# Optimization experiments

Measured on AMD Instinct MI355X. Metric: run time of the kernel, lower is better.

## Reference

```python
import jax, jax.numpy as jnp
import numpy as np

SR = 44100
N_BINS = 84
BPO = 12
FMIN = 32.7
HOP = 1024


def _config():
    # Static CQT geometry (mirrors ICQT.__init__)
    Q = 1.0 / (2.0 ** (1.0 / BPO) - 1.0)
    freqs = FMIN * 2.0 ** (np.arange(N_BINS) / BPO)
    wlens = np.round(Q * SR / freqs).astype(np.int64)  # per-bin window lengths (ragged)
    return freqs, wlens


def setup_inputs() -> dict:
    key = jax.random.key(0)
    # complex CQT stacked as (nb_samples, nb_channels, n_bins, n_frames, 2)
    X = jax.random.normal(key, (4, 2, N_BINS, 256, 2), dtype=jnp.float32)
    return {"X": X}


def reference(X):
    freqs, wlens = _config()
    max_wl = int(wlens.max())
    nb_s, nb_c, n_bins, n_frames, _ = X.shape
    # default length in ICQT.forward when length is None
    length = (n_frames - 1) * HOP + max_wl

    Xf = X.reshape(-1, n_bins, n_frames, 2)
    c = (Xf[..., 0] + 1j * Xf[..., 1]).astype(jnp.complex64)  # view_as_complex
    B = c.shape[0]

    starts = np.arange(n_frames) * HOP  # static frame start times
    out = jnp.zeros((B, length), jnp.float32)
    norm_np = np.zeros(length, np.float32)  # norm is input-independent -> static numpy

    for k in range(n_bins):  # fixed structural loop over ragged bins
        L = int(wlens[k])
        t = np.arange(L)
        # torch.hann_window(L) (periodic)
        win = (0.5 - 0.5 * np.cos(2.0 * np.pi * t / L)).astype(np.float32)
        omega = 2.0 * np.pi * float(freqs[k]) / SR
        # exp(+1j*omega*t) * window, fused into one basis vector
        basis = jnp.asarray((np.exp(1j * omega * t) * win).astype(np.complex64))
        # frames: (B, n_frames, L) = outer product of per-frame coeff and basis
        frames = c[:, k, :, None] * basis[None, None, :]
        # vectorized overlap-add scatter (duplicate indices accumulate)
        idx = (starts[:, None] + t[None, :]).reshape(-1)  # (n_frames*L,)
        out = out.at[:, idx].add(jnp.real(frames).reshape(B, -1))
        np.add.at(norm_np, idx, np.tile(win * win, n_frames))

    norm = jnp.asarray(np.where(norm_np > 1e-10, norm_np, 1.0).astype(np.float32))
    out = out / norm[None, :]
    return out.reshape(nb_s, nb_c, -1)
```

## Files before the change

### kernel.cpp

```cpp
#include <hip/hip_runtime.h>
#include <hip/hip_fp16.h>
#include <cmath>

#define NBINS   84
#define NFRAMES 256
#define HOP     1024
#define NB      8
#define KP      960
#define GBLK    278
#define MROWS   (GBLK*NB)
#define MPAD    2240
#define NRROWS  45

#define BT_BLOCKS   (4 * 1024)
#define A_BLOCKS    (4 * MPAD)
#define NORM_BLOCKS (NRROWS * 1024 / 4)
#define ALL_BLOCKS  (BT_BLOCKS + A_BLOCKS + NORM_BLOCKS)

typedef _Float16 f16x8 __attribute__((ext_vector_type(8)));
typedef float    f32x4 __attribute__((ext_vector_type(4)));

struct CqtArgs {
    int   wl[NBINS];
    float omega[NBINS];
    float invL[NBINS];
    int   Ktot;
    unsigned short ct[KP];
};

__global__ __launch_bounds__(256)
void mega_build(unsigned short* __restrict__ Am, unsigned short* __restrict__ Bt,
                float* __restrict__ NR, const float* __restrict__ X, CqtArgs a) {
    const int blk = blockIdx.x;
    const int tid = threadIdx.x;
    const float TWOPI = 6.28318530717958647692f;

    if (blk < BT_BLOCKS) {
        const int col = (blk & 3) * 256 + tid;
        const int r   = blk >> 2;
        if (col >= KP) return;
        float val = 0.f;
        const unsigned short rec = a.ct[col];
        if (rec != 0xFFFF) {
            const int k = rec & 0x7F, d = (rec >> 7) & 0x1F, c = rec >> 12;
            const int t = (d << 10) + r;
            if (t < a.wl[k]) {
                const float tf = (float)t;
                const float w  = 0.5f - 0.5f * cosf(TWOPI * tf * a.invL[k]);
                float s, cc;
                sincosf(a.omega[k] * tf, &s, &cc);
                val = (c ? s : cc) * w;
            }
        }
        Bt[(size_t)r * KP + col] = __half_as_ushort(__float2half(val));
    } else if (blk < BT_BLOCKS + A_BLOCKS) {
        const int idx = blk - BT_BLOCKS;
        const int col = (idx & 3) * 256 + tid;
        const int row = idx >> 2;
        if (col >= KP) return;
        float val = 0.f;
        const unsigned short rec = a.ct[col];
        if (row < MROWS && rec != 0xFFFF) {
            const int k = rec & 0x7F, d = (rec >> 7) & 0x1F, c = rec >> 12;
            const int g = row >> 3, b = row & 7;
            const int f = g - d;
            if (f >= 0 && f < NFRAMES) {
                const float x = X[(((size_t)b * NBINS + k) * NFRAMES + f) * 2 + c];
                val = c ? -x : x;
            }
        }
        Am[(size_t)row * KP + col] = __half_as_ushort(__float2half(val));
    } else {
        const int idx = blk - BT_BLOCKS - A_BLOCKS;
        const int w   = idx * 4 + (tid >> 6);
        const int l   = tid & 63;
        if (w >= NRROWS * 1024) return;
        const int grow = w >> 10;
        const int r    = w & 1023;
        const int g    = grow < 22 ? grow : (grow == 22 ? 128 : 233 + grow);

        float sum = 0.f;
        for (int j = l; j < KP / 2; j += 64) {
            const unsigned short rec = a.ct[2 * j];
            if (rec == 0xFFFF) continue;
            const int k = rec & 0x7F, d = (rec >> 7) & 0x1F;
            const int f = g - d;
            if (f < 0 || f >= NFRAMES) continue;
            const int t = (d << 10) + r;
            if (t < a.wl[k]) {
                const float wv = 0.5f - 0.5f * cosf(TWOPI * (float)t * a.invL[k]);
                sum += wv * wv;
            }
        }
#pragma unroll
        for (int off = 32; off; off >>= 1) sum += __shfl_xor(sum, off, 64);
        if (l == 0) NR[w] = (sum > 1e-10f) ? (1.0f / sum) : 1.0f;
    }
}

__global__ __launch_bounds__(256)
void gemm_icqt(const unsigned short* __restrict__ Am, const unsigned short* __restrict__ Bt,
               const float* __restrict__ NR, float* __restrict__ out, int length) {
    __shared__ __align__(16) char lds[16384];
    const int tid = threadIdx.x;
    const int l   = tid & 63;
    const int wid = tid >> 6;
    const int wm  = wid >> 1, wn = wid & 1;
    const int bm  = blockIdx.x, bn = blockIdx.y;

    const int q0 = tid,      q1 = tid + 256;
    const int r0 = q0 >> 3,  c0 = q0 & 7, s0 = c0 ^ (r0 & 7);
    const int r1 = q1 >> 3,  c1 = q1 & 7, s1 = c1 ^ (r1 & 7);

    const char* gA = (const char*)Am + (size_t)(bm * 64) * KP * 2;
    const char* gB = (const char*)Bt + (size_t)(bn * 64) * KP * 2;
    const char* gA0 = gA + ((size_t)r0 * KP + s0 * 8) * 2;
    const char* gA1 = gA + ((size_t)r1 * KP + s1 * 8) * 2;
    const char* gB0 = gB + ((size_t)r0 * KP + s0 * 8) * 2;
    const char* gB1 = gB + ((size_t)r1 * KP + s1 * 8) * 2;
    char* lA = lds;
    char* lB = lds + 8192;

    f32x4 acc00 = {0.f,0.f,0.f,0.f}, acc01 = {0.f,0.f,0.f,0.f};
    f32x4 acc10 = {0.f,0.f,0.f,0.f}, acc11 = {0.f,0.f,0.f,0.f};

    f16x8 ra0 = *(const f16x8*)(gA0);
    f16x8 ra1 = *(const f16x8*)(gA1);
    f16x8 rb0 = *(const f16x8*)(gB0);
    f16x8 rb1 = *(const f16x8*)(gB1);

    const int arow0 = wm * 32 + (l & 15), arow1 = arow0 + 16;
    const int brow0 = wn * 32 + (l & 15), brow1 = brow0 + 16;
    const int kq = l >> 4;

    for (int kk = 0; kk < KP; kk += 64) {
        __syncthreads();
        *(f16x8*)(lA + q0 * 16) = ra0;
        *(f16x8*)(lA + q1 * 16) = ra1;
        *(f16x8*)(lB + q0 * 16) = rb0;
        *(f16x8*)(lB + q1 * 16) = rb1;
        __syncthreads();
        if (kk + 64 < KP) {
            ra0 = *(const f16x8*)(gA0 + (kk + 64) * 2);
            ra1 = *(const f16x8*)(gA1 + (kk + 64) * 2);
            rb0 = *(const f16x8*)(gB0 + (kk + 64) * 2);
            rb1 = *(const f16x8*)(gB1 + (kk + 64) * 2);
        }
#pragma unroll
        for (int ks = 0; ks < 2; ++ks) {
            const int kb = ks * 4 + kq;
            f16x8 a0 = *(const f16x8*)(lA + arow0 * 128 + ((kb ^ (arow0 & 7)) << 4));
            f16x8 a1 = *(const f16x8*)(lA + arow1 * 128 + ((kb ^ (arow1 & 7)) << 4));
            f16x8 b0 = *(const f16x8*)(lB + brow0 * 128 + ((kb ^ (brow0 & 7)) << 4));
            f16x8 b1 = *(const f16x8*)(lB + brow1 * 128 + ((kb ^ (brow1 & 7)) << 4));
            acc00 = __builtin_amdgcn_mfma_f32_16x16x32_f16(a0, b0, acc00, 0, 0, 0);
            acc01 = __builtin_amdgcn_mfma_f32_16x16x32_f16(a0, b1, acc01, 0, 0, 0);
            acc10 = __builtin_amdgcn_mfma_f32_16x16x32_f16(a1, b0, acc10, 0, 0, 0);
            acc11 = __builtin_amdgcn_mfma_f32_16x16x32_f16(a1, b1, acc11, 0, 0, 0);
        }
    }

    const int mbase = bm * 64 + wm * 32;
    const int nbase = bn * 64 + wn * 32;
#pragma unroll
    for (int mi = 0; mi < 2; ++mi) {
#pragma unroll
        for (int ni = 0; ni < 2; ++ni) {
            f32x4 v = (mi == 0) ? ((ni == 0) ? acc00 : acc01)
                                : ((ni == 0) ? acc10 : acc11);
            const int ncol = nbase + ni * 16 + (l & 15);
#pragma unroll
            for (int reg = 0; reg < 4; ++reg) {
                const int mrow = mbase + mi * 16 + (l >> 4) * 4 + reg;
                if (mrow < MROWS) {
                    const int g = mrow >> 3, b = mrow & 7;
                    const int p = (g << 10) + ncol;
                    if (p < length) {
                        const int grow = (g < 22) ? g : ((g <= 255) ? 22 : g - 233);
                        out[(size_t)b * length + p] = v[reg] * NR[grow * 1024 + ncol];
                    }
                }
            }
        }
    }
}

__global__ void icqt_gather_fallback(const float* __restrict__ X, float* __restrict__ out,
                                     CqtArgs a, int length) {
    const int p = blockIdx.x * blockDim.x + threadIdx.x;
    if (p >= length) return;
    float acc[NB];
#pragma unroll
    for (int b = 0; b < NB; ++b) acc[b] = 0.0f;
    float nrm = 0.0f;
    int fhi = p >> 10;
    if (fhi > NFRAMES - 1) fhi = NFRAMES - 1;
    const float2* X2 = reinterpret_cast<const float2*>(X);
    for (int k = 0; k < NBINS; ++k) {
        const int L = a.wl[k];
        int flo = (p - L + HOP) >> 10;
        if (flo < 0) flo = 0;
        for (int f = flo; f <= fhi; ++f) {
            const int t = p - (f << 10);
            if (t < L) {
                float tf = (float)t;
                float ang = a.omega[k] * tf;
                float s = sinf(ang), c = cosf(ang);
                float w = 0.5f - 0.5f * cosf(6.28318530717958647692f * tf * a.invL[k]);
                float bre = c * w, bim = s * w;
                nrm += w * w;
                const int base = k * NFRAMES + f;
#pragma unroll
                for (int b = 0; b < NB; ++b) {
                    float2 cv = X2[(size_t)b * (NBINS * NFRAMES) + base];
                    acc[b] += cv.x * bre - cv.y * bim;
                }
            }
        }
    }
    const float inv = 1.0f / ((nrm > 1e-10f) ? nrm : 1.0f);
#pragma unroll
    for (int b = 0; b < NB; ++b)
        out[(size_t)b * length + p] = acc[b] * inv;
}

extern "C" void kernel_launch(void* const* d_in, const int* in_sizes, int n_in,
                              void* d_out, int out_size, void* d_ws, size_t ws_size,
                              hipStream_t stream) {
    CqtArgs a;
    int cb[NBINS];
    const double SR = 44100.0;
    const double Q  = 1.0 / (std::exp2(1.0 / 12.0) - 1.0);
    int Ktot = 0;
    for (int k = 0; k < NBINS; ++k) {
        double f = 32.7 * std::exp2((double)k / 12.0);
        int L = (int)std::nearbyint(Q * SR / f);
        a.wl[k]    = L;
        cb[k]      = Ktot;
        a.omega[k] = (float)(2.0 * 3.14159265358979323846 * f / SR);
        a.invL[k]  = (float)(1.0 / (double)L);
        Ktot += 2 * ((L + 1023) / 1024);
    }
    a.Ktot = Ktot;
    for (int col = 0; col < KP; ++col) a.ct[col] = 0xFFFF;
    if (Ktot <= KP) {
        for (int k = 0; k < NBINS; ++k) {
            const int D2 = 2 * ((a.wl[k] + 1023) / 1024);
            for (int j = 0; j < D2; ++j)
                a.ct[cb[k] + j] = (unsigned short)(k | ((j >> 1) << 7) | ((j & 1) << 12));
        }
    }

    const int length = out_size / NB;
    const float* X = (const float*)d_in[0];
    float* out     = (float*)d_out;

    const size_t offA  = 0;
    const size_t szA   = (size_t)MPAD * KP * 2;
    const size_t offB  = offA + szA;
    const size_t szB   = (size_t)1024 * KP * 2;
    const size_t offNR = offB + szB;
    const size_t szNR  = (size_t)NRROWS * 1024 * 4;
    const size_t need  = offNR + szNR;

    if (Ktot > KP || ws_size < need) {
        const int blocks = (length + 255) / 256;
        icqt_gather_fallback<<<blocks, 256, 0, stream>>>(X, out, a, length);
        return;
    }

    unsigned short* Am = (unsigned short*)((char*)d_ws + offA);
    unsigned short* Bt = (unsigned short*)((char*)d_ws + offB);
    float*          NR = (float*)((char*)d_ws + offNR);

    mega_build<<<dim3(ALL_BLOCKS), 256, 0, stream>>>(Am, Bt, NR, X, a);
    gemm_icqt<<<dim3(MPAD / 64, 1024 / 64), 256, 0, stream>>>(Am, Bt, NR, out, length);
}
```

Before: 52.62 us.

## Compute norm via per-sample window-square prefix and pack complex pairs in build

The normalization table is no longer built by per-row reductions over all columns. Instead, the build kernel computes S[t], the sum of squared Hann windows over bins at each window offset t, and the GEMM epilogue sums the few overlapping frame shifts per output to form the inverse norm. The A and B build paths now handle real/imag column pairs together, doing one sincos and one float2 load and writing packed 32-bit half pairs, which halves the block count. This moves some norm work into the GEMM epilogue and adds a fallback condition on window length.

```diff
diff --git a/kernel.cpp b/kernel.cpp
--- a/kernel.cpp
+++ b/kernel.cpp
@@ -7,15 +7,16 @@
 #define HOP     1024
 #define NB      8
 #define KP      960
+#define KPH     (KP/2)
 #define GBLK    278
 #define MROWS   (GBLK*NB)
 #define MPAD    2240
-#define NRROWS  45
-
-#define BT_BLOCKS   (4 * 1024)
-#define A_BLOCKS    (4 * MPAD)
-#define NORM_BLOCKS (NRROWS * 1024 / 4)
-#define ALL_BLOCKS  (BT_BLOCKS + A_BLOCKS + NORM_BLOCKS)
+#define SD      23
+
+#define BT_BLOCKS  2048
+#define A_BLOCKS   (2*MPAD)
+#define S_BLOCKS   92
+#define ALL_BLOCKS (BT_BLOCKS + A_BLOCKS + S_BLOCKS)
 
 typedef _Float16 f16x8 __attribute__((ext_vector_type(8)));
 typedef float    f32x4 __attribute__((ext_vector_type(4)));
@@ -30,77 +31,72 @@
 
 __global__ __launch_bounds__(256)
 void mega_build(unsigned short* __restrict__ Am, unsigned short* __restrict__ Bt,
-                float* __restrict__ NR, const float* __restrict__ X, CqtArgs a) {
+                float* __restrict__ S, const float* __restrict__ X, CqtArgs a) {
     const int blk = blockIdx.x;
     const int tid = threadIdx.x;
     const float TWOPI = 6.28318530717958647692f;
 
     if (blk < BT_BLOCKS) {
-        const int col = (blk & 3) * 256 + tid;
-        const int r   = blk >> 2;
-        if (col >= KP) return;
-        float val = 0.f;
-        const unsigned short rec = a.ct[col];
+        const int r = blk >> 1;
+        const int j = (blk & 1) * 256 + tid;
+        if (j >= KPH) return;
+        unsigned int pack = 0;
+        const unsigned short rec = a.ct[2 * j];
         if (rec != 0xFFFF) {
-            const int k = rec & 0x7F, d = (rec >> 7) & 0x1F, c = rec >> 12;
+            const int k = rec & 0x7F, d = (rec >> 7) & 0x1F;
             const int t = (d << 10) + r;
             if (t < a.wl[k]) {
                 const float tf = (float)t;
                 const float w  = 0.5f - 0.5f * cosf(TWOPI * tf * a.invL[k]);
-                float s, cc;
-                sincosf(a.omega[k] * tf, &s, &cc);
-                val = (c ? s : cc) * w;
-            }
-        }
-        Bt[(size_t)r * KP + col] = __half_as_ushort(__float2half(val));
+                float s, c;
+                sincosf(a.omega[k] * tf, &s, &c);
+                pack = (unsigned int)__half_as_ushort(__float2half(c * w))
+                     | ((unsigned int)__half_as_ushort(__float2half(s * w)) << 16);
+            }
+        }
+        *(unsigned int*)(Bt + (size_t)r * KP + 2 * j) = pack;
     } else if (blk < BT_BLOCKS + A_BLOCKS) {
         const int idx = blk - BT_BLOCKS;
-        const int col = (idx & 3) * 256 + tid;
-        const int row = idx >> 2;
-        if (col >= KP) return;
-        float val = 0.f;
-        const unsigned short rec = a.ct[col];
+        const int row = idx >> 1;
+        const int j   = (idx & 1) * 256 + tid;
+        if (j >= KPH) return;
+        unsigned int pack = 0;
+        const unsigned short rec = a.ct[2 * j];
         if (row < MROWS && rec != 0xFFFF) {
-            const int k = rec & 0x7F, d = (rec >> 7) & 0x1F, c = rec >> 12;
+            const int k = rec & 0x7F, d = (rec >> 7) & 0x1F;
             const int g = row >> 3, b = row & 7;
             const int f = g - d;
             if (f >= 0 && f < NFRAMES) {
-                const float x = X[(((size_t)b * NBINS + k) * NFRAMES + f) * 2 + c];
-                val = c ? -x : x;
-            }
-        }
-        Am[(size_t)row * KP + col] = __half_as_ushort(__float2half(val));
+                const float2 x = *(const float2*)(X + (((size_t)b * NBINS + k) * NFRAMES + f) * 2);
+                pack = (unsigned int)__half_as_ushort(__float2half(x.x))
+                     | ((unsigned int)__half_as_ushort(__float2half(-x.y)) << 16);
+            }
+        }
+        *(unsigned int*)(Am + (size_t)row * KP + 2 * j) = pack;
     } else {
-        const int idx = blk - BT_BLOCKS - A_BLOCKS;
-        const int w   = idx * 4 + (tid >> 6);
-        const int l   = tid & 63;
-        if (w >= NRROWS * 1024) return;
-        const int grow = w >> 10;
-        const int r    = w & 1023;
-        const int g    = grow < 22 ? grow : (grow == 22 ? 128 : 233 + grow);
-
+        const int t = (blk - BT_BLOCKS - A_BLOCKS) * 256 + tid;
         float sum = 0.f;
-        for (int j = l; j < KP / 2; j += 64) {
-            const unsigned short rec = a.ct[2 * j];
-            if (rec == 0xFFFF) continue;
-            const int k = rec & 0x7F, d = (rec >> 7) & 0x1F;
-            const int f = g - d;
-            if (f < 0 || f >= NFRAMES) continue;
-            const int t = (d << 10) + r;
-            if (t < a.wl[k]) {
-                const float wv = 0.5f - 0.5f * cosf(TWOPI * (float)t * a.invL[k]);
-                sum += wv * wv;
-            }
-        }
-#pragma unroll
-        for (int off = 32; off; off >>= 1) sum += __shfl_xor(sum, off, 64);
-        if (l == 0) NR[w] = (sum > 1e-10f) ? (1.0f / sum) : 1.0f;
-    }
+        for (int k = 0; k < NBINS; ++k) {
+            if (t >= a.wl[k]) break;
+            const float w = 0.5f - 0.5f * cosf(TWOPI * (float)t * a.invL[k]);
+            sum += w * w;
+        }
+        S[t] = sum;
+    }
+}
+
+__device__ __forceinline__ float inv_norm(const float* __restrict__ S, int g, int ncol) {
+    if (g >= GBLK) return 1.0f;
+    const int lo = (g > NFRAMES - 1) ? (g - (NFRAMES - 1)) : 0;
+    const int hi = g < (SD - 1) ? g : (SD - 1);
+    float s = 0.f;
+    for (int d = lo; d <= hi; ++d) s += S[(d << 10) + ncol];
+    return (s > 1e-10f) ? 1.0f / s : 1.0f;
 }
 
 __global__ __launch_bounds__(256)
 void gemm_icqt(const unsigned short* __restrict__ Am, const unsigned short* __restrict__ Bt,
-               const float* __restrict__ NR, float* __restrict__ out, int length) {
+               const float* __restrict__ S, float* __restrict__ out, int length) {
     __shared__ __align__(16) char lds[16384];
     const int tid = threadIdx.x;
     const int l   = tid & 63;
@@ -162,23 +158,31 @@
 
     const int mbase = bm * 64 + wm * 32;
     const int nbase = bn * 64 + wn * 32;
+    const int ncol0 = nbase + (l & 15);
+    const int ncol1 = ncol0 + 16;
+    const int g0    = (mbase >> 3) + (kq >> 1);
+    const float inv00 = inv_norm(S, g0,     ncol0);
+    const float inv01 = inv_norm(S, g0,     ncol1);
+    const float inv10 = inv_norm(S, g0 + 2, ncol0);
+    const float inv11 = inv_norm(S, g0 + 2, ncol1);
+
 #pragma unroll
     for (int mi = 0; mi < 2; ++mi) {
 #pragma unroll
         for (int ni = 0; ni < 2; ++ni) {
             f32x4 v = (mi == 0) ? ((ni == 0) ? acc00 : acc01)
                                 : ((ni == 0) ? acc10 : acc11);
-            const int ncol = nbase + ni * 16 + (l & 15);
+            const float invv = (mi == 0) ? ((ni == 0) ? inv00 : inv01)
+                                         : ((ni == 0) ? inv10 : inv11);
+            const int ncol = (ni == 0) ? ncol0 : ncol1;
 #pragma unroll
             for (int reg = 0; reg < 4; ++reg) {
-                const int mrow = mbase + mi * 16 + (l >> 4) * 4 + reg;
+                const int mrow = mbase + mi * 16 + kq * 4 + reg;
                 if (mrow < MROWS) {
                     const int g = mrow >> 3, b = mrow & 7;
                     const int p = (g << 10) + ncol;
-                    if (p < length) {
-                        const int grow = (g < 22) ? g : ((g <= 255) ? 22 : g - 233);
-                        out[(size_t)b * length + p] = v[reg] * NR[grow * 1024 + ncol];
-                    }
+                    if (p < length)
+                        out[(size_t)b * length + p] = v[reg] * invv;
                 }
             }
         }
@@ -255,15 +259,15 @@
     const float* X = (const float*)d_in[0];
     float* out     = (float*)d_out;
 
-    const size_t offA  = 0;
-    const size_t szA   = (size_t)MPAD * KP * 2;
-    const size_t offB  = offA + szA;
-    const size_t szB   = (size_t)1024 * KP * 2;
-    const size_t offNR = offB + szB;
-    const size_t szNR  = (size_t)NRROWS * 1024 * 4;
-    const size_t need  = offNR + szNR;
-
-    if (Ktot > KP || ws_size < need) {
+    const size_t offA = 0;
+    const size_t szA  = (size_t)MPAD * KP * 2;
+    const size_t offB = offA + szA;
+    const size_t szB  = (size_t)1024 * KP * 2;
+    const size_t offS = offB + szB;
+    const size_t szS  = (size_t)SD * 1024 * 4;
+    const size_t need = offS + szS;
+
+    if (Ktot > KP || a.wl[0] > SD * 1024 || ws_size < need) {
         const int blocks = (length + 255) / 256;
         icqt_gather_fallback<<<blocks, 256, 0, stream>>>(X, out, a, length);
         return;
@@ -271,8 +275,8 @@
 
     unsigned short* Am = (unsigned short*)((char*)d_ws + offA);
     unsigned short* Bt = (unsigned short*)((char*)d_ws + offB);
-    float*          NR = (float*)((char*)d_ws + offNR);
-
-    mega_build<<<dim3(ALL_BLOCKS), 256, 0, stream>>>(Am, Bt, NR, X, a);
-    gemm_icqt<<<dim3(MPAD / 64, 1024 / 64), 256, 0, stream>>>(Am, Bt, NR, out, length);
-}
+    float*          S  = (float*)((char*)d_ws + offS);
+
+    mega_build<<<dim3(ALL_BLOCKS), 256, 0, stream>>>(Am, Bt, S, X, a);
+    gemm_icqt<<<dim3(MPAD / 64, 1024 / 64), 256, 0, stream>>>(Am, Bt, S, out, length);
+}
```

Result: no change. 53.29 us (+1.3%).
